# Optimization experiments

Measured on AMD Instinct MI355X. Metric: run time of the kernel, lower is better.

The kernel has to match this reference:

```python
import jax, jax.numpy as jnp
import numpy as np
import itertools

N_SET = 4        # number of elements in the input set (input.size(-2))
IN_F = 2048      # in_features
OUT_F = 2048     # out_features
BOT = 512        # bottleneck_dim
B = 512          # batch size
NUM_NODES = 391
EMB_DIM = 300

# All nonempty subsets of range(N_SET), ordered by scale then lexicographic,
# exactly matching the torch loop over scales / itertools.combinations.
SUBSETS = [c for s in range(1, N_SET + 1) for c in itertools.combinations(range(N_SET), s)]

def _incl_matrix():
    # M[i, j] = 1 if SUBSETS[j] is a subset of SUBSETS[i].
    # This reproduces the dict-based scatter-sum: the aggregated output for rset
    # is the sum of raw Relation outputs over all nonempty k \subseteq rset.
    masks = [sum(1 << i for i in c) for c in SUBSETS]
    n = len(masks)
    M = np.zeros((n, n), dtype=np.float32)
    for i, mi in enumerate(masks):
        for j, mj in enumerate(masks):
            if (mj & mi) == mj:
                M[i, j] = 1.0
    return M

INCL = _incl_matrix()  # [15, 15]

def setup_inputs():
    key = jax.random.key(0)
    ks = jax.random.split(key, 16)
    inp = {"x": jax.random.normal(ks[0], (B, N_SET, IN_F), dtype=jnp.float32)}
    ki = 1
    for s in range(1, N_SET + 1):
        fan = s * IN_F
        inp[f"w1_s{s}"] = jax.random.normal(ks[ki], (BOT, fan), dtype=jnp.float32) / np.float32(np.sqrt(fan)); ki += 1
        inp[f"b1_s{s}"] = jnp.zeros((BOT,), dtype=jnp.float32)
        inp[f"w2_s{s}"] = jax.random.normal(ks[ki], (OUT_F, BOT), dtype=jnp.float32) / np.float32(np.sqrt(BOT)); ki += 1
        inp[f"b2_s{s}"] = jnp.zeros((OUT_F,), dtype=jnp.float32)
    inp["w_emb"] = jax.random.normal(ks[ki], (EMB_DIM, OUT_F), dtype=jnp.float32) / np.float32(np.sqrt(OUT_F)); ki += 1
    inp["b_emb"] = jnp.zeros((EMB_DIM,), dtype=jnp.float32)
    inp["w_node"] = jax.random.normal(ks[ki], (NUM_NODES, OUT_F), dtype=jnp.float32) / np.float32(np.sqrt(OUT_F)); ki += 1
    inp["b_node"] = jnp.zeros((NUM_NODES,), dtype=jnp.float32)
    return inp

def _base_forward(x, ws):
    # Batched per-scale Relation MLPs over all C(4,s) subsets at once.
    raws = []
    for s in range(1, N_SET + 1):
        idx = np.array(list(itertools.combinations(range(N_SET), s)))  # [C, s]
        g = x[:, idx, :]                                  # [B, C, s, F] gather
        h = g.reshape(g.shape[0], g.shape[1], s * IN_F)   # concat along subset
        w1, b1, w2, b2 = ws[s - 1]
        h = jax.nn.relu(h)
        h = jax.nn.relu(jnp.einsum('bcf,of->bco', h, w1) + b1)
        raws.append(jnp.einsum('bcd,od->bco', h, w2) + b2)  # [B, C, OUT_F]
    raw = jnp.concatenate(raws, axis=1)  # [B, 15, OUT_F]
    # Subset-inclusion scatter-sum, expressed as a dense 15x15 contraction.
    return jnp.einsum('ij,bjf->bif', jnp.asarray(INCL), raw)

def reference(x, w1_s1, b1_s1, w2_s1, b2_s1, w1_s2, b1_s2, w2_s2, b2_s2,
              w1_s3, b1_s3, w2_s3, b2_s3, w1_s4, b1_s4, w2_s4, b2_s4,
              w_emb, b_emb, w_node, b_node):
    ws = [(w1_s1, b1_s1, w2_s1, b2_s1), (w1_s2, b1_s2, w2_s2, b2_s2),
          (w1_s3, b1_s3, w2_s3, b2_s3), (w1_s4, b1_s4, w2_s4, b2_s4)]
    feats = _base_forward(x, ws)                              # [B, 15, OUT_F]
    embeddings = jnp.einsum('bnf,ef->bne', feats, w_emb) + b_emb  # [B, 15, 300]
    node_out = jnp.einsum('bnf,vf->bnv', feats, w_node) + b_node  # [B, 15, 391]
    return embeddings, jnp.swapaxes(node_out, -2, -1)             # [B, 391, 15]
```

## Files before the change

### kernel.cpp

```cpp
#include <hip/hip_runtime.h>
#include <stdint.h>

using bf16x8 = __attribute__((ext_vector_type(8))) short;
using f32x4  = __attribute__((ext_vector_type(4))) float;

#define DEVINL __device__ __forceinline__

DEVINL unsigned short f2bf(float f) {
  union { float f; unsigned u; } v; v.f = f;
  unsigned u = v.u;
  return (unsigned short)((u + 0x7FFFu + ((u >> 16) & 1u)) >> 16);
}
DEVINL float bf2f(unsigned short h) {
  union { unsigned u; float f; } v; v.u = ((unsigned)h) << 16;
  return v.f;
}

DEVINL void gload_lds16(const void* g, void* l) {
  __builtin_amdgcn_global_load_lds(
      (const __attribute__((address_space(1))) void*)g,
      (__attribute__((address_space(3))) void*)l, 16, 0, 0);
}

template<int OUT_BF16, int HAS_BIAS>
DEVINL void gemm_core(const unsigned short* __restrict__ A,
                      const unsigned short* __restrict__ B,
                      void* __restrict__ C,
                      const float* __restrict__ bias,
                      int K, int Cld, int arow0, int brow0, int crow0, int ccol0)
{
  __shared__ __align__(16) unsigned short As[2][256 * 64];
  __shared__ __align__(16) unsigned short Bs[2][128 * 64];

  const int t    = threadIdx.x;
  const int wave = t >> 6;
  const int lane = t & 63;
  const int wr   = (wave >> 1) << 6;
  const int wc   = (wave & 1) << 6;
  const int lrow = lane & 15;
  const int kg   = lane >> 4;

  f32x4 acc[4][4];
#pragma unroll
  for (int r = 0; r < 4; ++r)
#pragma unroll
    for (int q = 0; q < 4; ++q) acc[r][q] = (f32x4){0.f, 0.f, 0.f, 0.f};

  const int srow = t >> 3;
  const int scol = (((t & 7) ^ (srow & 7)) << 3);
  const unsigned short* aSrc = A + (size_t)(arow0 + srow) * K + scol;
  const unsigned short* bSrc = B + (size_t)(brow0 + srow) * K + scol;

  const int nt = K >> 6;
  {
    char* aD = (char*)As[0] + wave * 1024;
    char* bD = (char*)Bs[0] + wave * 1024;
#pragma unroll
    for (int p = 0; p < 4; ++p)
      gload_lds16(aSrc + (size_t)(p * 64) * K, aD + p * 8192);
#pragma unroll
    for (int p = 0; p < 2; ++p)
      gload_lds16(bSrc + (size_t)(p * 64) * K, bD + p * 8192);
  }
  const int rs = lrow & 7;
  const int cA0 = ((kg + 0) ^ rs) << 3;
  const int cA1 = ((kg + 4) ^ rs) << 3;

  int cur = 0;
  for (int tt = 0; tt < nt; ++tt) {
    if (tt + 1 < nt) {
      const int k0 = (tt + 1) << 6;
      char* aD = (char*)As[cur ^ 1] + wave * 1024;
      char* bD = (char*)Bs[cur ^ 1] + wave * 1024;
#pragma unroll
      for (int p = 0; p < 4; ++p)
        gload_lds16(aSrc + (size_t)(p * 64) * K + k0, aD + p * 8192);
#pragma unroll
      for (int p = 0; p < 2; ++p)
        gload_lds16(bSrc + (size_t)(p * 64) * K + k0, bD + p * 8192);
      asm volatile("s_waitcnt vmcnt(6)" ::: "memory");
    } else {
      asm volatile("s_waitcnt vmcnt(0)" ::: "memory");
    }
    asm volatile("s_barrier" ::: "memory");
    const unsigned short* Ab = As[cur];
    const unsigned short* Bb = Bs[cur];
#pragma unroll
    for (int kk = 0; kk < 64; kk += 32) {
      const int cofs = (kk == 0) ? cA0 : cA1;
      bf16x8 af[4], bq[4];
#pragma unroll
      for (int r = 0; r < 4; ++r)
        af[r] = *(const bf16x8*)&Ab[(wr + r * 16 + lrow) * 64 + cofs];
#pragma unroll
      for (int q = 0; q < 4; ++q)
        bq[q] = *(const bf16x8*)&Bb[(wc + q * 16 + lrow) * 64 + cofs];
#pragma unroll
      for (int r = 0; r < 4; ++r)
#pragma unroll
        for (int q = 0; q < 4; ++q)
          acc[r][q] = __builtin_amdgcn_mfma_f32_16x16x32_bf16(af[r], bq[q], acc[r][q], 0, 0, 0);
    }
    asm volatile("s_barrier" ::: "memory");
    cur ^= 1;
  }

#pragma unroll
  for (int r = 0; r < 4; ++r) {
#pragma unroll
    for (int q = 0; q < 4; ++q) {
      const int col = ccol0 + wc + q * 16 + lrow;
      const float bv = HAS_BIAS ? bias[col] : 0.f;
#pragma unroll
      for (int v = 0; v < 4; ++v) {
        const int row = crow0 + wr + r * 16 + (kg << 2) + v;
        const float val = acc[r][q][v] + bv;
        if (OUT_BF16)
          ((unsigned short*)C)[(size_t)row * Cld + col] = f2bf(val);
        else
          ((float*)C)[(size_t)row * Cld + col] = val;
      }
    }
  }
}

__global__ __launch_bounds__(512) void mega1_k(const unsigned short* __restrict__ xrb,
                                               const unsigned short* __restrict__ w1cat,
                                               const unsigned short* __restrict__ wen,
                                               const unsigned short* __restrict__ w2t,
                                               unsigned short* __restrict__ H0p,
                                               unsigned short* __restrict__ W2EN) {
  const int bid = blockIdx.x;
  if (bid < 160) {
    const int p = bid >> 3, q = bid & 7;
    const int rt = q >> 2, ct = q & 3;
    const int MM[20] = {0,1,2,3, 0,1,2, 1,2,3, 0,1, 1,2, 2,3, 0,1,2,3};
    const int JJ[20] = {0,0,0,0, 1,1,1, 2,2,2, 3,3, 4,4, 5,5, 6,7,8,9};
    gemm_core<1, 0>(xrb, w1cat, H0p, nullptr, 2048, 512,
                    MM[p] * 512 + rt * 256, JJ[p] * 512 + ct * 128,
                    p * 512 + rt * 256, ct * 128);
  } else {
    const int b2 = bid - 160;
    const int s = b2 / 12, r = b2 % 12;
    const int rt = r >> 2, ct = r & 3;
    gemm_core<1, 0>(wen, w2t, W2EN, nullptr, 2048, 512,
                    rt * 256, s * 512 + ct * 128,
                    s * 768 + rt * 256, ct * 128);
  }
}

__global__ __launch_bounds__(512) void gemmF_k(const unsigned short* __restrict__ h1,
                                               const unsigned short* __restrict__ W2EN,
                                               const float* __restrict__ ENb,
                                               float* __restrict__ EN0) {
  const int y = blockIdx.y;
  const int c = y >> 1;
  const int s = (c < 4) ? 1 : (c < 10) ? 2 : (c < 14) ? 3 : 4;
  gemm_core<0, 1>(h1, W2EN, EN0, ENb + (size_t)(s - 1) * 768, 512, 768,
                  y * 256, (s - 1) * 768 + blockIdx.x * 128,
                  y * 256, blockIdx.x * 128);
}

__global__ __launch_bounds__(256) void prep_all_k(const float* __restrict__ x,
                                                  const float* w11, const float* w12,
                                                  const float* w13, const float* w14,
                                                  const float* w21, const float* w22,
                                                  const float* w23, const float* w24,
                                                  const float* __restrict__ wemb,
                                                  const float* __restrict__ wnode,
                                                  const float* b21, const float* b22,
                                                  const float* b23, const float* b24,
                                                  unsigned short* __restrict__ xrb,
                                                  unsigned short* __restrict__ w1cat,
                                                  unsigned short* __restrict__ w2t,
                                                  unsigned short* __restrict__ wen,
                                                  float* __restrict__ ENb) {
  __shared__ float lds[64][65];
  __shared__ float red[4][4];
  const int bid = blockIdx.x;
  if (bid < 10240) {
    const int tid = bid * 256 + threadIdx.x;
    const int r = tid >> 9;
    const int k = (tid & 511) << 2;
    const int j = r >> 9, o = r & 511;
    const float* src; int s, tt;
    if (j == 0)      { src = w11; s = 1; tt = 0; }
    else if (j < 3)  { src = w12; s = 2; tt = j - 1; }
    else if (j < 6)  { src = w13; s = 3; tt = j - 3; }
    else             { src = w14; s = 4; tt = j - 6; }
    const float4 vv = *(const float4*)(src + (size_t)o * (s * 2048) + tt * 2048 + k);
    ushort4 ov;
    ov.x = f2bf(vv.x); ov.y = f2bf(vv.y); ov.z = f2bf(vv.z); ov.w = f2bf(vv.w);
    *(ushort4*)(w1cat + (size_t)r * 2048 + k) = ov;
  } else if (bid < 14336) {
    const int tid = (bid - 10240) * 256 + threadIdx.x;
    const int r = tid >> 9;
    const int k = (tid & 511) << 2;
    const int m = r >> 9, b = r & 511;
    const float4 vv = *(const float4*)(x + ((size_t)(b * 4 + m)) * 2048 + k);
    ushort4 o;
    o.x = f2bf(fmaxf(vv.x, 0.f)); o.y = f2bf(fmaxf(vv.y, 0.f));
    o.z = f2bf(fmaxf(vv.z, 0.f)); o.w = f2bf(fmaxf(vv.w, 0.f));
    *(ushort4*)(xrb + (size_t)r * 2048 + k) = o;
  } else if (bid < 15360) {
    const int idx = bid - 14336;
    const int s = idx >> 8, rem = idx & 255;
    const int rt = rem >> 3, ct = rem & 7;
    const float* src = (s == 0) ? w21 : (s == 1) ? w22 : (s == 2) ? w23 : w24;
    const int tr = threadIdx.x >> 4;
    const int tc = (threadIdx.x & 15) << 2;
#pragma unroll
    for (int i = 0; i < 4; ++i) {
      const float4 v = *(const float4*)(src + (size_t)(rt * 64 + tr + 16 * i) * 512 + ct * 64 + tc);
      lds[tr + 16 * i][tc + 0] = v.x; lds[tr + 16 * i][tc + 1] = v.y;
      lds[tr + 16 * i][tc + 2] = v.z; lds[tr + 16 * i][tc + 3] = v.w;
    }
    __syncthreads();
#pragma unroll
    for (int i = 0; i < 4; ++i) {
      ushort4 ov;
      ov.x = f2bf(lds[tc + 0][tr + 16 * i]); ov.y = f2bf(lds[tc + 1][tr + 16 * i]);
      ov.z = f2bf(lds[tc + 2][tr + 16 * i]); ov.w = f2bf(lds[tc + 3][tr + 16 * i]);
      *(ushort4*)(w2t + ((size_t)s * 512 + ct * 64 + tr + 16 * i) * 2048 + rt * 64 + tc) = ov;
    }
  } else if (bid < 16896) {
    const int tid = (bid - 15360) * 256 + threadIdx.x;
    const int r = tid >> 9;
    const int k = (tid & 511) << 2;
    float4 vv = make_float4(0.f, 0.f, 0.f, 0.f);
    if (r < 300)       vv = *(const float4*)(wemb + (size_t)r * 2048 + k);
    else if (r < 691)  vv = *(const float4*)(wnode + (size_t)(r - 300) * 2048 + k);
    ushort4 ov;
    ov.x = f2bf(vv.x); ov.y = f2bf(vv.y); ov.z = f2bf(vv.z); ov.w = f2bf(vv.w);
    *(ushort4*)(wen + (size_t)r * 2048 + k) = ov;
  } else {
    const int e = bid - 16896;
    const int t8 = threadIdx.x << 3;
    float a0 = 0.f, a1 = 0.f, a2 = 0.f, a3 = 0.f;
    if (e < 691) {
      const float* row = (e < 300) ? (wemb + (size_t)e * 2048)
                                   : (wnode + (size_t)(e - 300) * 2048);
      const float4 r0 = *(const float4*)(row + t8);
      const float4 r1 = *(const float4*)(row + t8 + 4);
      const float4 c10 = *(const float4*)(b21 + t8), c11 = *(const float4*)(b21 + t8 + 4);
      const float4 c20 = *(const float4*)(b22 + t8), c21 = *(const float4*)(b22 + t8 + 4);
      const float4 c30 = *(const float4*)(b23 + t8), c31 = *(const float4*)(b23 + t8 + 4);
      const float4 c40 = *(const float4*)(b24 + t8), c41 = *(const float4*)(b24 + t8 + 4);
      a0 = r0.x*c10.x + r0.y*c10.y + r0.z*c10.z + r0.w*c10.w
         + r1.x*c11.x + r1.y*c11.y + r1.z*c11.z + r1.w*c11.w;
      a1 = r0.x*c20.x + r0.y*c20.y + r0.z*c20.z + r0.w*c20.w
         + r1.x*c21.x + r1.y*c21.y + r1.z*c21.z + r1.w*c21.w;
      a2 = r0.x*c30.x + r0.y*c30.y + r0.z*c30.z + r0.w*c30.w
         + r1.x*c31.x + r1.y*c31.y + r1.z*c31.z + r1.w*c31.w;
      a3 = r0.x*c40.x + r0.y*c40.y + r0.z*c40.z + r0.w*c40.w
         + r1.x*c41.x + r1.y*c41.y + r1.z*c41.z + r1.w*c41.w;
    }
#pragma unroll
    for (int off = 32; off; off >>= 1) {
      a0 += __shfl_down(a0, off); a1 += __shfl_down(a1, off);
      a2 += __shfl_down(a2, off); a3 += __shfl_down(a3, off);
    }
    const int wv = threadIdx.x >> 6;
    if ((threadIdx.x & 63) == 0) {
      red[wv][0] = a0; red[wv][1] = a1; red[wv][2] = a2; red[wv][3] = a3;
    }
    __syncthreads();
    if (threadIdx.x < 4) {
      const float v = red[0][threadIdx.x] + red[1][threadIdx.x] +
                      red[2][threadIdx.x] + red[3][threadIdx.x];
      ENb[(size_t)threadIdx.x * 768 + e] = (e < 691) ? v : 0.f;
    }
  }
}

__global__ __launch_bounds__(128) void combine1_k(const unsigned short* __restrict__ H0p,
                                                  unsigned short* __restrict__ h1,
                                                  const float* __restrict__ b11,
                                                  const float* __restrict__ b12,
                                                  const float* __restrict__ b13,
                                                  const float* __restrict__ b14) {
  const int cb = blockIdx.x;
  const int c = cb >> 9, b = cb & 511;
  const int s = (c < 4) ? 1 : (c < 10) ? 2 : (c < 14) ? 3 : 4;
  const unsigned char P[15][4] = {
    {0,0,0,0},{1,0,0,0},{2,0,0,0},{3,0,0,0},
    {4,7,0,0},{4,8,0,0},{4,9,0,0},{5,8,0,0},{5,9,0,0},{6,9,0,0},
    {10,12,14,0},{10,12,15,0},{10,13,15,0},{11,13,15,0},
    {16,17,18,19}};
  const float* b1 = (s == 1) ? b11 : (s == 2) ? b12 : (s == 3) ? b13 : b14;
  const int o = threadIdx.x << 2;
  float4 a = *(const float4*)(b1 + o);
  for (int t = 0; t < s; ++t) {
    const int p = P[c][t];
    const ushort4 hv = *(const ushort4*)(H0p + ((size_t)(p * 512 + b)) * 512 + o);
    a.x += bf2f(hv.x); a.y += bf2f(hv.y); a.z += bf2f(hv.z); a.w += bf2f(hv.w);
  }
  ushort4 ov;
  ov.x = f2bf(fmaxf(a.x, 0.f)); ov.y = f2bf(fmaxf(a.y, 0.f));
  ov.z = f2bf(fmaxf(a.z, 0.f)); ov.w = f2bf(fmaxf(a.w, 0.f));
  *(ushort4*)(h1 + (size_t)cb * 512 + o) = ov;
}

__global__ __launch_bounds__(256) void combine2_k(const float* __restrict__ EN0,
                                                  const float* __restrict__ b_emb,
                                                  const float* __restrict__ b_node,
                                                  float* __restrict__ out0,
                                                  float* __restrict__ out1) {
  const int b   = blockIdx.x;
  const int col = blockIdx.y * 256 + threadIdx.x;
  if (col >= 691) return;
  float vals[15];
#pragma unroll
  for (int j = 0; j < 15; ++j)
    vals[j] = EN0[((size_t)(j * 512 + b)) * 768 + col];
  const int MSK[15] = {1,2,4,8,3,5,9,6,10,12,7,11,13,14,15};
  if (col < 300) {
    const float be = b_emb[col];
#pragma unroll
    for (int i = 0; i < 15; ++i) {
      float sum = be;
#pragma unroll
      for (int j = 0; j < 15; ++j)
        if ((MSK[j] & MSK[i]) == MSK[j]) sum += vals[j];
      out0[((size_t)b * 15 + i) * 300 + col] = sum;
    }
  } else {
    const int v = col - 300;
    const float bn = b_node[v];
#pragma unroll
    for (int i = 0; i < 15; ++i) {
      float sum = bn;
#pragma unroll
      for (int j = 0; j < 15; ++j)
        if ((MSK[j] & MSK[i]) == MSK[j]) sum += vals[j];
      out1[((size_t)b * 391 + v) * 15 + i] = sum;
    }
  }
}

extern "C" void kernel_launch(void* const* d_in, const int* in_sizes, int n_in,
                              void* d_out, int out_size, void* d_ws, size_t ws_size,
                              hipStream_t stream) {
  const float* x     = (const float*)d_in[0];
  const float* w11   = (const float*)d_in[1];
  const float* b11   = (const float*)d_in[2];
  const float* w21   = (const float*)d_in[3];
  const float* b21   = (const float*)d_in[4];
  const float* w12   = (const float*)d_in[5];
  const float* b12   = (const float*)d_in[6];
  const float* w22   = (const float*)d_in[7];
  const float* b22   = (const float*)d_in[8];
  const float* w13   = (const float*)d_in[9];
  const float* b13   = (const float*)d_in[10];
  const float* w23   = (const float*)d_in[11];
  const float* b23   = (const float*)d_in[12];
  const float* w14   = (const float*)d_in[13];
  const float* b14   = (const float*)d_in[14];
  const float* w24   = (const float*)d_in[15];
  const float* b24   = (const float*)d_in[16];
  const float* wemb  = (const float*)d_in[17];
  const float* bemb  = (const float*)d_in[18];
  const float* wnode = (const float*)d_in[19];
  const float* bnode = (const float*)d_in[20];

  char* ws = (char*)d_ws;
  unsigned short* xrb   = (unsigned short*)(ws + 0);
  unsigned short* w1cat = (unsigned short*)(ws + 8388608);
  unsigned short* w2t   = (unsigned short*)(ws + 29360128);
  unsigned short* wen   = (unsigned short*)(ws + 37748736);
  unsigned short* H0p   = (unsigned short*)(ws + 40894464);
  unsigned short* W2EN  = (unsigned short*)(ws + 51380224);
  float*          ENb   = (float*)(ws + 54525952);
  unsigned short* h1bf  = (unsigned short*)(ws + 54538240);
  float*          EN0   = (float*)(ws + 0);

  float* out0 = (float*)d_out;
  float* out1 = out0 + 2304000;

  prep_all_k<<<17664, 256, 0, stream>>>(x, w11, w12, w13, w14, w21, w22, w23, w24,
                                        wemb, wnode, b21, b22, b23, b24,
                                        xrb, w1cat, w2t, wen, ENb);
  mega1_k   <<<208, 512, 0, stream>>>(xrb, w1cat, wen, w2t, H0p, W2EN);
  combine1_k<<<7680, 128, 0, stream>>>(H0p, h1bf, b11, b12, b13, b14);
  gemmF_k   <<<dim3(6, 30), 512, 0, stream>>>(h1bf, W2EN, ENb, EN0);
  combine2_k<<<dim3(512, 3), 256, 0, stream>>>(EN0, bemb, bnode, out0, out1);
}
```

Before: 99.10 us.

## Triple-buffer GEMM LDS tiles and interleave MFMA with LDS reads using setprio

Moves the shared GEMM core from double to triple buffering, so global-to-LDS loads run two K-tiles ahead with a deeper vmcnt wait. The inner loop is reorganised into four phases separated by barriers, where LDS fragment reads for the second half-tile overlap MFMA work on the first, and s_setprio raises wave priority around the MFMA bursts. The aim is to hide global and LDS latency behind matrix math. The cost is LDS use rising from 96KB to 144KB per block, which may cut occupancy, plus extra barriers each iteration.

```diff
diff --git a/kernel.cpp b/kernel.cpp
--- a/kernel.cpp
+++ b/kernel.cpp
@@ -29,8 +29,8 @@
                       const float* __restrict__ bias,
                       int K, int Cld, int arow0, int brow0, int crow0, int ccol0)
 {
-  __shared__ __align__(16) unsigned short As[2][256 * 64];
-  __shared__ __align__(16) unsigned short Bs[2][128 * 64];
+  __shared__ __align__(16) unsigned short As[3][256 * 64];
+  __shared__ __align__(16) unsigned short Bs[3][128 * 64];
 
   const int t    = threadIdx.x;
   const int wave = t >> 6;
@@ -51,58 +51,87 @@
   const unsigned short* aSrc = A + (size_t)(arow0 + srow) * K + scol;
   const unsigned short* bSrc = B + (size_t)(brow0 + srow) * K + scol;
 
+  auto STAGE = [&](int slot, int kt) {
+    const int k0 = kt << 6;
+    char* aD = (char*)As[slot] + wave * 1024;
+    char* bD = (char*)Bs[slot] + wave * 1024;
+#pragma unroll
+    for (int p = 0; p < 4; ++p)
+      gload_lds16(aSrc + (size_t)(p * 64) * K + k0, aD + p * 8192);
+#pragma unroll
+    for (int p = 0; p < 2; ++p)
+      gload_lds16(bSrc + (size_t)(p * 64) * K + k0, bD + p * 8192);
+  };
+
   const int nt = K >> 6;
-  {
-    char* aD = (char*)As[0] + wave * 1024;
-    char* bD = (char*)Bs[0] + wave * 1024;
-#pragma unroll
-    for (int p = 0; p < 4; ++p)
-      gload_lds16(aSrc + (size_t)(p * 64) * K, aD + p * 8192);
-#pragma unroll
-    for (int p = 0; p < 2; ++p)
-      gload_lds16(bSrc + (size_t)(p * 64) * K, bD + p * 8192);
-  }
+  STAGE(0, 0);
+  STAGE(1, 1);
+
   const int rs = lrow & 7;
   const int cA0 = ((kg + 0) ^ rs) << 3;
   const int cA1 = ((kg + 4) ^ rs) << 3;
 
-  int cur = 0;
-  for (int tt = 0; tt < nt; ++tt) {
-    if (tt + 1 < nt) {
-      const int k0 = (tt + 1) << 6;
-      char* aD = (char*)As[cur ^ 1] + wave * 1024;
-      char* bD = (char*)Bs[cur ^ 1] + wave * 1024;
-#pragma unroll
-      for (int p = 0; p < 4; ++p)
-        gload_lds16(aSrc + (size_t)(p * 64) * K + k0, aD + p * 8192);
-#pragma unroll
-      for (int p = 0; p < 2; ++p)
-        gload_lds16(bSrc + (size_t)(p * 64) * K + k0, bD + p * 8192);
+  int sl = 0;
+  for (int kt = 0; kt < nt; ++kt) {
+    const unsigned short* Ab = As[sl];
+    const unsigned short* Bb = Bs[sl];
+    if (kt + 2 < nt) {
+      int s2 = sl + 2; if (s2 >= 3) s2 -= 3;
+      STAGE(s2, kt + 2);
+      asm volatile("s_waitcnt vmcnt(12)" ::: "memory");
+    } else if (kt + 1 < nt) {
       asm volatile("s_waitcnt vmcnt(6)" ::: "memory");
     } else {
       asm volatile("s_waitcnt vmcnt(0)" ::: "memory");
     }
-    asm volatile("s_barrier" ::: "memory");
-    const unsigned short* Ab = As[cur];
-    const unsigned short* Bb = Bs[cur];
-#pragma unroll
-    for (int kk = 0; kk < 64; kk += 32) {
-      const int cofs = (kk == 0) ? cA0 : cA1;
-      bf16x8 af[4], bq[4];
-#pragma unroll
-      for (int r = 0; r < 4; ++r)
-        af[r] = *(const bf16x8*)&Ab[(wr + r * 16 + lrow) * 64 + cofs];
+    __builtin_amdgcn_s_barrier();
+
+    bf16x8 a0[4], b0[4], a1[4], b1[4];
+#pragma unroll
+    for (int r = 0; r < 4; ++r)
+      a0[r] = *(const bf16x8*)&Ab[(wr + r * 16 + lrow) * 64 + cA0];
+#pragma unroll
+    for (int q = 0; q < 4; ++q)
+      b0[q] = *(const bf16x8*)&Bb[(wc + q * 16 + lrow) * 64 + cA0];
+    __builtin_amdgcn_s_setprio(1);
+#pragma unroll
+    for (int r = 0; r < 2; ++r)
 #pragma unroll
       for (int q = 0; q < 4; ++q)
-        bq[q] = *(const bf16x8*)&Bb[(wc + q * 16 + lrow) * 64 + cofs];
-#pragma unroll
-      for (int r = 0; r < 4; ++r)
-#pragma unroll
-        for (int q = 0; q < 4; ++q)
-          acc[r][q] = __builtin_amdgcn_mfma_f32_16x16x32_bf16(af[r], bq[q], acc[r][q], 0, 0, 0);
-    }
-    asm volatile("s_barrier" ::: "memory");
-    cur ^= 1;
+        acc[r][q] = __builtin_amdgcn_mfma_f32_16x16x32_bf16(a0[r], b0[q], acc[r][q], 0, 0, 0);
+    __builtin_amdgcn_s_setprio(0);
+    __builtin_amdgcn_s_barrier();
+#pragma unroll
+    for (int r = 0; r < 4; ++r)
+      a1[r] = *(const bf16x8*)&Ab[(wr + r * 16 + lrow) * 64 + cA1];
+#pragma unroll
+    for (int q = 0; q < 4; ++q)
+      b1[q] = *(const bf16x8*)&Bb[(wc + q * 16 + lrow) * 64 + cA1];
+    __builtin_amdgcn_s_setprio(1);
+#pragma unroll
+    for (int r = 2; r < 4; ++r)
+#pragma unroll
+      for (int q = 0; q < 4; ++q)
+        acc[r][q] = __builtin_amdgcn_mfma_f32_16x16x32_bf16(a0[r], b0[q], acc[r][q], 0, 0, 0);
+    __builtin_amdgcn_s_setprio(0);
+    __builtin_amdgcn_s_barrier();
+    __builtin_amdgcn_s_setprio(1);
+#pragma unroll
+    for (int r = 0; r < 2; ++r)
+#pragma unroll
+      for (int q = 0; q < 4; ++q)
+        acc[r][q] = __builtin_amdgcn_mfma_f32_16x16x32_bf16(a1[r], b1[q], acc[r][q], 0, 0, 0);
+    __builtin_amdgcn_s_setprio(0);
+    __builtin_amdgcn_s_barrier();
+    __builtin_amdgcn_s_setprio(1);
+#pragma unroll
+    for (int r = 2; r < 4; ++r)
+#pragma unroll
+      for (int q = 0; q < 4; ++q)
+        acc[r][q] = __builtin_amdgcn_mfma_f32_16x16x32_bf16(a1[r], b1[q], acc[r][q], 0, 0, 0);
+    __builtin_amdgcn_s_setprio(0);
+    __builtin_amdgcn_s_barrier();
+    ++sl; if (sl == 3) sl = 0;
   }
 
 #pragma unroll
```

Result: slower. 105.9 us (+6.9%).
